# Optimization experiments

Hardware: AMD Instinct MI355X
Metric: run time of the kernel (lower is better)

Reference implementation:

```python
import jax, jax.numpy as jnp
import numpy as np

N_HEAD = 16
MAX_SEQ_LEN = 2048
RATIO = 1
NEG_INF = -jnp.inf


def make_alibi_bias(n_head: int, max_seq_len: int, ratio: int) -> jnp.ndarray:
    # bias[t, s] = s*ratio - t, masked to -inf where > 0 (future positions)
    s = jnp.arange(max_seq_len)[None, :] * ratio            # [1, S]
    t = jnp.arange(max_seq_len * ratio)[:, None]            # [T, 1]
    bias = (s - t).astype(jnp.float32)                      # [T, S]
    bias = jnp.where(bias > 0, NEG_INF, bias)
    # per-head slopes: cumprod of 2^(-8/n_head) -> m_i = 2^(-8*(i+1)/n_head)
    m = jnp.cumprod(jnp.full((n_head,), 2.0 ** (-8.0 / n_head), dtype=jnp.float32))
    return bias[None, :, :] * m[:, None, None]              # [H, T, S]


def setup_inputs() -> dict:
    key = jax.random.key(0)
    kq, kk, kv = jax.random.split(key, 3)
    B, T, D = 2, 2048, 1024
    return {
        "q": jax.random.normal(kq, (B, T, D), dtype=jnp.float32),
        "k": jax.random.normal(kk, (B, T, D), dtype=jnp.float32),
        "v": jax.random.normal(kv, (B, T, D), dtype=jnp.float32),
    }


def reference(q, k, v):
    B, T, D = q.shape
    S = k.shape[1]
    H = N_HEAD
    dh = D // H
    # split heads: [B, T, D] -> [B, H, T, dh]
    qh = q.reshape(B, T, H, dh).transpose(0, 2, 1, 3)
    kh = k.reshape(B, S, H, dh).transpose(0, 2, 1, 3)
    vh = v.reshape(B, S, H, dh).transpose(0, 2, 1, 3)

    scores = jnp.einsum("bhtd,bhsd->bhts", qh, kh) / jnp.sqrt(jnp.float32(dh))
    bias = make_alibi_bias(H, MAX_SEQ_LEN, RATIO)[:, -T:, -S:]  # [H, T, S]
    attn = jax.nn.softmax(scores + bias[None], axis=-1)
    out = jnp.einsum("bhts,bhsd->bhtd", attn, vh)
    # gather heads: [B, H, T, dh] -> [B, T, D]
    return out.transpose(0, 2, 1, 3).reshape(B, T, D)
```

## Files before the change

### kernel.cpp

```cpp
#include <hip/hip_runtime.h>

#define N_HEAD 16
#define DHEAD 64
#define TSEQ 2048
#define DMODEL 1024
#define BATCH 2

typedef _Float16 f16x8 __attribute__((ext_vector_type(8)));
typedef _Float16 f16x4 __attribute__((ext_vector_type(4)));
typedef _Float16 f16x2 __attribute__((ext_vector_type(2)));
typedef __fp16 fp16x2 __attribute__((ext_vector_type(2)));
typedef float f32x4 __attribute__((ext_vector_type(4)));

union F8 { f16x8 v; uint4 u; f16x2 h[4]; };
union F4 { f16x4 v; uint2 u; f16x2 h[2]; };

#if __has_builtin(__builtin_amdgcn_exp2f)
#define EXP2F(x) __builtin_amdgcn_exp2f(x)
#else
#define EXP2F(x) exp2f(x)
#endif

__device__ __forceinline__ void gload_lds16(const void* g, void* l) {
    __builtin_amdgcn_global_load_lds(
        (const __attribute__((address_space(1))) void*)g,
        (__attribute__((address_space(3))) void*)l, 16, 0, 0);
}

__device__ __forceinline__ f16x2 pk(float a, float b) {
    union { fp16x2 i; f16x2 o; } c;
    c.i = __builtin_amdgcn_cvt_pkrtz(a, b);
    return c.o;
}

__device__ __forceinline__ F8 pack8_f32(const float* p) {
    const float4 a = *(const float4*)p;
    const float4 b = *(const float4*)(p + 4);
    F8 r;
    r.h[0] = pk(a.x, a.y); r.h[1] = pk(a.z, a.w);
    r.h[2] = pk(b.x, b.y); r.h[3] = pk(b.z, b.w);
    return r;
}

__global__ __launch_bounds__(256) void prep(const float* __restrict__ K,
                                            const float* __restrict__ V,
                                            _Float16* __restrict__ Kh,
                                            _Float16* __restrict__ Vh)
{
    __shared__ float tl[64][67];
    const int bh = blockIdx.y, b = bh >> 4, h = bh & 15;
    const int s0 = blockIdx.x * 64;
    const int t = threadIdx.x;
    const int r16 = t >> 4, c4 = (t & 15) * 4;
    #pragma unroll
    for (int pass = 0; pass < 4; ++pass) {
        const int row = pass * 16 + r16;
        const size_t goff = ((size_t)(b * TSEQ + s0 + row)) * DMODEL + h * DHEAD + c4;
        const float4 fk = *(const float4*)(K + goff);
        F4 ok;
        ok.h[0] = pk(fk.x, fk.y);
        ok.h[1] = pk(fk.z, fk.w);
        *(uint2*)(Kh + (((size_t)bh * TSEQ + s0 + row) << 6) + c4) = ok.u;
        const float4 fv = *(const float4*)(V + goff);
        tl[row][c4 + 0] = fv.x; tl[row][c4 + 1] = fv.y;
        tl[row][c4 + 2] = fv.z; tl[row][c4 + 3] = fv.w;
    }
    __syncthreads();
    const int d = t >> 2, sc = (t & 3) * 16;
    F8 p0, p1;
    #pragma unroll
    for (int j = 0; j < 4; ++j) p0.h[j] = pk(tl[sc + 2 * j][d], tl[sc + 2 * j + 1][d]);
    #pragma unroll
    for (int j = 0; j < 4; ++j) p1.h[j] = pk(tl[sc + 8 + 2 * j][d], tl[sc + 9 + 2 * j][d]);
    _Float16* vo = Vh + ((size_t)bh * DHEAD + d) * TSEQ + s0 + sc;
    *(uint4*)vo = p0.u;
    *(uint4*)(vo + 8) = p1.u;
}

__global__ __launch_bounds__(256, 4) void alibi_attn(
    const float* __restrict__ Q, const _Float16* __restrict__ Kh,
    const _Float16* __restrict__ Vh, float* __restrict__ O)
{
    __shared__ __align__(16) char kbuf[2][8192];
    __shared__ __align__(16) char vbuf[2][8192];

    const int wv   = threadIdx.x >> 6;
    const int lane = threadIdx.x & 63;
    const int quad = lane >> 4;
    const int l16  = lane & 15;

    const int bh = blockIdx.x;
    const int b  = bh >> 4, h = bh & 15;
    const int sx = 31 - (int)blockIdx.y;

    const float LOG2E   = 1.44269504088896f;
    const float slope   = exp2f(-0.5f * (float)(h + 1));
    const float bslope2 = slope * LOG2E;
    const float sscale2 = 0.125f * LOG2E;
    const float step64  = 64.0f * bslope2;
    const float rb1 = bslope2, rb2 = 2.f * bslope2, rb3 = 3.f * bslope2;

    const float* qp  = Q + (size_t)b * TSEQ * DMODEL + (size_t)h * DHEAD;
    const char*  kpb = (const char*)(Kh + (size_t)bh * TSEQ * DHEAD);
    const char*  vpb = (const char*)(Vh + (size_t)bh * DHEAD * TSEQ);

    const int st_r  = lane >> 3;
    const int k_src = st_r * 128  + (((lane & 7) ^ st_r) * 16);
    const int v_src = st_r * 4096 + (((lane & 7) ^ st_r) * 16);

    const int koff0 = l16 * 128 + ((quad ^ (l16 & 7)) * 16);
    const int koff1 = l16 * 128 + (((quad + 4) ^ (l16 & 7)) * 16);
    const int vbase = l16 * 128 + (quad & 1) * 8;
    int vx[4];
    #pragma unroll
    for (int sj = 0; sj < 4; ++sj)
        vx[sj] = ((sj * 2 + (quad >> 1)) ^ (l16 & 7)) * 16;

    const f32x4 zero4 = {0.f, 0.f, 0.f, 0.f};

    const int base_w = sx * 64 + wv * 16;

    auto stage = [&](int t) {
        const char* kg = kpb + (size_t)t * 8192;
        const char* vg = vpb + (size_t)t * 128;
        char* kd = kbuf[t & 1];
        char* vd = vbuf[t & 1];
        #pragma unroll
        for (int c = 0; c < 2; ++c) {
            const int gr = wv * 16 + c * 8;
            gload_lds16(kg + gr * 128 + k_src, kd + gr * 128);
            gload_lds16(vg + gr * 4096 + v_src, vd + gr * 128);
        }
    };

    stage(0);

    const float* qr = qp + (size_t)(base_w + l16) * DMODEL + quad * 8;
    const F8 aq0 = pack8_f32(qr);
    const F8 aq1 = pack8_f32(qr + 32);

    f32x4 o[4];
    float lp = 0.f;
    float dbq[4];
    #pragma unroll
    for (int nt = 0; nt < 4; ++nt) o[nt] = zero4;
    #pragma unroll
    for (int sj = 0; sj < 4; ++sj)
        dbq[sj] = (float)(sj * 16 + quad * 4 - base_w - l16) * bslope2;

    __syncthreads();

    for (int t = 0; t <= sx; ++t) {
        if (t < sx) stage(t + 1);
        const char* kb = kbuf[t & 1];
        const char* vb = vbuf[t & 1];

        F8 kA[4][2];
        #pragma unroll
        for (int sj = 0; sj < 4; ++sj) {
            kA[sj][0].u = *(const uint4*)(kb + sj * 2048 + koff0);
            kA[sj][1].u = *(const uint4*)(kb + sj * 2048 + koff1);
        }

        f32x4 sT[4];
        #pragma unroll
        for (int sj = 0; sj < 4; ++sj) {
            f32x4 acc = zero4;
            acc = __builtin_amdgcn_mfma_f32_16x16x32_f16(kA[sj][0].v, aq0.v, acc, 0, 0, 0);
            acc = __builtin_amdgcn_mfma_f32_16x16x32_f16(kA[sj][1].v, aq1.v, acc, 0, 0, 0);
            sT[sj] = acc;
        }

        F4 vf[4][4];
        #pragma unroll
        for (int nt = 0; nt < 4; ++nt)
            #pragma unroll
            for (int sj = 0; sj < 4; ++sj)
                vf[nt][sj].u = *(const uint2*)(vb + nt * 2048 + vbase + vx[sj]);

        const bool masked = (t == sx);
        F4 pP[4];
        #pragma unroll
        for (int sj = 0; sj < 4; ++sj) {
            const float db = dbq[sj];
            float p0 = EXP2F(fmaf(sT[sj][0], sscale2, db));
            float p1 = EXP2F(fmaf(sT[sj][1], sscale2, db + rb1));
            float p2 = EXP2F(fmaf(sT[sj][2], sscale2, db + rb2));
            float p3 = EXP2F(fmaf(sT[sj][3], sscale2, db + rb3));
            if (masked) {
                const int di = t * 64 + sj * 16 + quad * 4 - base_w - l16;
                if (di + 0 > 0) p0 = 0.f;
                if (di + 1 > 0) p1 = 0.f;
                if (di + 2 > 0) p2 = 0.f;
                if (di + 3 > 0) p3 = 0.f;
            }
            lp += (p0 + p1) + (p2 + p3);
            pP[sj].h[0] = pk(p0, p1);
            pP[sj].h[1] = pk(p2, p3);
            dbq[sj] = db + step64;
        }

        #pragma unroll
        for (int nt = 0; nt < 4; ++nt)
            #pragma unroll
            for (int sj = 0; sj < 4; ++sj)
                o[nt] = __builtin_amdgcn_mfma_f32_16x16x16f16(
                    pP[sj].v, vf[nt][sj].v, o[nt], 0, 0, 0);

        __syncthreads();
    }

    float ls = lp;
    ls += __shfl_xor(ls, 16);
    ls += __shfl_xor(ls, 32);
    float lr[4];
    #pragma unroll
    for (int r = 0; r < 4; ++r)
        lr[r] = __shfl(ls, quad * 4 + r);
    #pragma unroll
    for (int nt = 0; nt < 4; ++nt)
        #pragma unroll
        for (int r = 0; r < 4; ++r) {
            const int trow = base_w + quad * 4 + r;
            O[((size_t)b * TSEQ + trow) * DMODEL + h * DHEAD + nt * 16 + l16] =
                o[nt][r] / lr[r];
        }
}

extern "C" void kernel_launch(void* const* d_in, const int* in_sizes, int n_in,
                              void* d_out, int out_size, void* d_ws, size_t ws_size,
                              hipStream_t stream) {
    const float* q = (const float*)d_in[0];
    const float* k = (const float*)d_in[1];
    const float* v = (const float*)d_in[2];
    float* out = (float*)d_out;

    _Float16* Kh = (_Float16*)d_ws;
    _Float16* Vh = Kh + (size_t)BATCH * N_HEAD * TSEQ * DHEAD;

    prep<<<dim3(TSEQ / 64, BATCH * N_HEAD), 256, 0, stream>>>(k, v, Kh, Vh);
    alibi_attn<<<dim3(BATCH * N_HEAD, 32), 256, 0, stream>>>(q, Kh, Vh, out);
}
```

Baseline: 126.8 us.

## Split key tiles across waves instead of query rows, reduce partials via LDS

Restructures the attention block so each wave processes all 64 query rows against its own 16-key slice of each key tile, rather than each wave owning 16 query rows over all keys. This cuts per-wave LDS reads of K/V fragments fourfold. The cost is a cross-wave reduction of output partials and row sums through shared memory at the end, plus four times the accumulator registers, so launch bounds drop to 2 blocks per SM. It also adds s_setprio around MFMA sections.

After: 127.9 us. About the same (+0.8%).

```diff
diff --git a/kernel.cpp b/kernel.cpp
--- a/kernel.cpp
+++ b/kernel.cpp
@@ -77,12 +77,13 @@
     *(uint4*)(vo + 8) = p1.u;
 }
 
-__global__ __launch_bounds__(256, 4) void alibi_attn(
+__global__ __launch_bounds__(256, 2) void alibi_attn(
     const float* __restrict__ Q, const _Float16* __restrict__ Kh,
     const _Float16* __restrict__ Vh, float* __restrict__ O)
 {
-    __shared__ __align__(16) char kbuf[2][8192];
-    __shared__ __align__(16) char vbuf[2][8192];
+    __shared__ __align__(16) char smem[32768];
+    char* kb0 = smem;
+    char* vb0 = smem + 16384;
 
     const int wv   = threadIdx.x >> 6;
     const int lane = threadIdx.x & 63;
@@ -91,7 +92,8 @@
 
     const int bh = blockIdx.x;
     const int b  = bh >> 4, h = bh & 15;
-    const int sx = 31 - (int)blockIdx.y;
+    const int qt = 31 - (int)blockIdx.y;
+    const int sx = qt;
 
     const float LOG2E   = 1.44269504088896f;
     const float slope   = exp2f(-0.5f * (float)(h + 1));
@@ -111,20 +113,15 @@
     const int koff0 = l16 * 128 + ((quad ^ (l16 & 7)) * 16);
     const int koff1 = l16 * 128 + (((quad + 4) ^ (l16 & 7)) * 16);
     const int vbase = l16 * 128 + (quad & 1) * 8;
-    int vx[4];
-    #pragma unroll
-    for (int sj = 0; sj < 4; ++sj)
-        vx[sj] = ((sj * 2 + (quad >> 1)) ^ (l16 & 7)) * 16;
+    const int vxw   = ((wv * 2 + (quad >> 1)) ^ (l16 & 7)) * 16;
 
     const f32x4 zero4 = {0.f, 0.f, 0.f, 0.f};
-
-    const int base_w = sx * 64 + wv * 16;
 
     auto stage = [&](int t) {
         const char* kg = kpb + (size_t)t * 8192;
         const char* vg = vpb + (size_t)t * 128;
-        char* kd = kbuf[t & 1];
-        char* vd = vbuf[t & 1];
+        char* kd = kb0 + (t & 1) * 8192;
+        char* vd = vb0 + (t & 1) * 8192;
         #pragma unroll
         for (int c = 0; c < 2; ++c) {
             const int gr = wv * 16 + c * 8;
@@ -135,96 +132,154 @@
 
     stage(0);
 
-    const float* qr = qp + (size_t)(base_w + l16) * DMODEL + quad * 8;
-    const F8 aq0 = pack8_f32(qr);
-    const F8 aq1 = pack8_f32(qr + 32);
-
-    f32x4 o[4];
-    float lp = 0.f;
+    F8 aq[4][2];
+    #pragma unroll
+    for (int qb = 0; qb < 4; ++qb) {
+        const float* qr = qp + (size_t)(qt * 64 + qb * 16 + l16) * DMODEL + quad * 8;
+        aq[qb][0] = pack8_f32(qr);
+        aq[qb][1] = pack8_f32(qr + 32);
+    }
+
+    f32x4 o[4][4];
+    float lp[4];
     float dbq[4];
     #pragma unroll
-    for (int nt = 0; nt < 4; ++nt) o[nt] = zero4;
-    #pragma unroll
-    for (int sj = 0; sj < 4; ++sj)
-        dbq[sj] = (float)(sj * 16 + quad * 4 - base_w - l16) * bslope2;
+    for (int qb = 0; qb < 4; ++qb) {
+        #pragma unroll
+        for (int nt = 0; nt < 4; ++nt) o[qb][nt] = zero4;
+        lp[qb] = 0.f;
+        dbq[qb] = (float)(wv * 16 + quad * 4 - qt * 64 - qb * 16 - l16) * bslope2;
+    }
 
     __syncthreads();
 
     for (int t = 0; t <= sx; ++t) {
         if (t < sx) stage(t + 1);
-        const char* kb = kbuf[t & 1];
-        const char* vb = vbuf[t & 1];
-
-        F8 kA[4][2];
-        #pragma unroll
-        for (int sj = 0; sj < 4; ++sj) {
-            kA[sj][0].u = *(const uint4*)(kb + sj * 2048 + koff0);
-            kA[sj][1].u = *(const uint4*)(kb + sj * 2048 + koff1);
-        }
+        const char* kb = kb0 + (t & 1) * 8192;
+        const char* vb = vb0 + (t & 1) * 8192;
+
+        F8 kA0, kA1;
+        kA0.u = *(const uint4*)(kb + wv * 2048 + koff0);
+        kA1.u = *(const uint4*)(kb + wv * 2048 + koff1);
+
+        F4 vf[4];
+        #pragma unroll
+        for (int nt = 0; nt < 4; ++nt)
+            vf[nt].u = *(const uint2*)(vb + nt * 2048 + vbase + vxw);
 
         f32x4 sT[4];
-        #pragma unroll
-        for (int sj = 0; sj < 4; ++sj) {
+        __builtin_amdgcn_s_setprio(1);
+        #pragma unroll
+        for (int qb = 0; qb < 4; ++qb) {
             f32x4 acc = zero4;
-            acc = __builtin_amdgcn_mfma_f32_16x16x32_f16(kA[sj][0].v, aq0.v, acc, 0, 0, 0);
-            acc = __builtin_amdgcn_mfma_f32_16x16x32_f16(kA[sj][1].v, aq1.v, acc, 0, 0, 0);
-            sT[sj] = acc;
-        }
-
-        F4 vf[4][4];
-        #pragma unroll
-        for (int nt = 0; nt < 4; ++nt)
-            #pragma unroll
-            for (int sj = 0; sj < 4; ++sj)
-                vf[nt][sj].u = *(const uint2*)(vb + nt * 2048 + vbase + vx[sj]);
+            acc = __builtin_amdgcn_mfma_f32_16x16x32_f16(kA0.v, aq[qb][0].v, acc, 0, 0, 0);
+            acc = __builtin_amdgcn_mfma_f32_16x16x32_f16(kA1.v, aq[qb][1].v, acc, 0, 0, 0);
+            sT[qb] = acc;
+        }
+        __builtin_amdgcn_s_setprio(0);
 
         const bool masked = (t == sx);
         F4 pP[4];
         #pragma unroll
-        for (int sj = 0; sj < 4; ++sj) {
-            const float db = dbq[sj];
-            float p0 = EXP2F(fmaf(sT[sj][0], sscale2, db));
-            float p1 = EXP2F(fmaf(sT[sj][1], sscale2, db + rb1));
-            float p2 = EXP2F(fmaf(sT[sj][2], sscale2, db + rb2));
-            float p3 = EXP2F(fmaf(sT[sj][3], sscale2, db + rb3));
+        for (int qb = 0; qb < 4; ++qb) {
+            const float db = dbq[qb];
+            float p0 = EXP2F(fmaf(sT[qb][0], sscale2, db));
+            float p1 = EXP2F(fmaf(sT[qb][1], sscale2, db + rb1));
+            float p2 = EXP2F(fmaf(sT[qb][2], sscale2, db + rb2));
+            float p3 = EXP2F(fmaf(sT[qb][3], sscale2, db + rb3));
             if (masked) {
-                const int di = t * 64 + sj * 16 + quad * 4 - base_w - l16;
+                const int di = t * 64 + wv * 16 + quad * 4 - (qt * 64 + qb * 16 + l16);
                 if (di + 0 > 0) p0 = 0.f;
                 if (di + 1 > 0) p1 = 0.f;
                 if (di + 2 > 0) p2 = 0.f;
                 if (di + 3 > 0) p3 = 0.f;
             }
-            lp += (p0 + p1) + (p2 + p3);
-            pP[sj].h[0] = pk(p0, p1);
-            pP[sj].h[1] = pk(p2, p3);
-            dbq[sj] = db + step64;
-        }
-
-        #pragma unroll
-        for (int nt = 0; nt < 4; ++nt)
+            lp[qb] += (p0 + p1) + (p2 + p3);
+            pP[qb].h[0] = pk(p0, p1);
+            pP[qb].h[1] = pk(p2, p3);
+            dbq[qb] = db + step64;
+        }
+
+        __builtin_amdgcn_s_setprio(1);
+        #pragma unroll
+        for (int qb = 0; qb < 4; ++qb)
             #pragma unroll
-            for (int sj = 0; sj < 4; ++sj)
-                o[nt] = __builtin_amdgcn_mfma_f32_16x16x16f16(
-                    pP[sj].v, vf[nt][sj].v, o[nt], 0, 0, 0);
+            for (int nt = 0; nt < 4; ++nt)
+                o[qb][nt] = __builtin_amdgcn_mfma_f32_16x16x16f16(
+                    pP[qb].v, vf[nt].v, o[qb][nt], 0, 0, 0);
+        __builtin_amdgcn_s_setprio(0);
 
         __syncthreads();
     }
 
-    float ls = lp;
-    ls += __shfl_xor(ls, 16);
-    ls += __shfl_xor(ls, 32);
-    float lr[4];
-    #pragma unroll
-    for (int r = 0; r < 4; ++r)
-        lr[r] = __shfl(ls, quad * 4 + r);
-    #pragma unroll
-    for (int nt = 0; nt < 4; ++nt)
-        #pragma unroll
-        for (int r = 0; r < 4; ++r) {
-            const int trow = base_w + quad * 4 + r;
-            O[((size_t)b * TSEQ + trow) * DMODEL + h * DHEAD + nt * 16 + l16] =
-                o[nt][r] / lr[r];
-        }
+    float lsq[4];
+    #pragma unroll
+    for (int qb = 0; qb < 4; ++qb) {
+        float ls = lp[qb];
+        ls += __shfl_xor(ls, 16);
+        ls += __shfl_xor(ls, 32);
+        lsq[qb] = ls;
+    }
+    float* lred = (float*)smem;
+    if (quad == 0) {
+        #pragma unroll
+        for (int qb = 0; qb < 4; ++qb)
+            lred[wv * 64 + qb * 16 + l16] = lsq[qb];
+    }
+    __syncthreads();
+
+    const int tt   = threadIdx.x;
+    const int qb2  = tt >> 7;
+    const int qrow = (tt >> 3) & 15;
+    const int chnk = tt & 7;
+    float lA = 0.f, lB = 0.f;
+    #pragma unroll
+    for (int w = 0; w < 4; ++w) {
+        lA += lred[w * 64 + qb2 * 16 + qrow];
+        lB += lred[w * 64 + (2 + qb2) * 16 + qrow];
+    }
+    __syncthreads();
+
+    float* part = (float*)smem;
+    #pragma unroll
+    for (int R = 0; R < 2; ++R) {
+        #pragma unroll
+        for (int q2 = 0; q2 < 2; ++q2) {
+            const int qb = R * 2 + q2;
+            #pragma unroll
+            for (int nt = 0; nt < 4; ++nt) {
+                const int cd = nt * 2 + (l16 >> 3);
+                #pragma unroll
+                for (int r = 0; r < 4; ++r) {
+                    const int q  = quad * 4 + r;
+                    const int cs = cd ^ (q & 7);
+                    part[((wv * 2 + q2) * 16 + q) * 64 + cs * 8 + (l16 & 7)] =
+                        o[qb][nt][r];
+                }
+            }
+        }
+        __syncthreads();
+
+        const float lf = R ? lB : lA;
+        const int cs = chnk ^ (qrow & 7);
+        float r0[8] = {0, 0, 0, 0, 0, 0, 0, 0};
+        #pragma unroll
+        for (int w = 0; w < 4; ++w) {
+            const float* pp = &part[((w * 2 + qb2) * 16 + qrow) * 64 + cs * 8];
+            const float4 a = *(const float4*)pp;
+            const float4 c = *(const float4*)(pp + 4);
+            r0[0] += a.x; r0[1] += a.y; r0[2] += a.z; r0[3] += a.w;
+            r0[4] += c.x; r0[5] += c.y; r0[6] += c.z; r0[7] += c.w;
+        }
+        const int qg = qt * 64 + (R * 2 + qb2) * 16 + qrow;
+        float* op = O + ((size_t)b * TSEQ + qg) * DMODEL + h * DHEAD + chnk * 8;
+        const float inv = 1.f / lf;
+        float4 w0 = {r0[0] * inv, r0[1] * inv, r0[2] * inv, r0[3] * inv};
+        float4 w1 = {r0[4] * inv, r0[5] * inv, r0[6] * inv, r0[7] * inv};
+        *(float4*)op = w0;
+        *(float4*)(op + 4) = w1;
+        __syncthreads();
+    }
 }
 
 extern "C" void kernel_launch(void* const* d_in, const int* in_sizes, int n_in,
```
